# Performance work log

Hardware: AMD Instinct MI355X
Metric: run time of the kernel (lower is better)

## Reference

```python
import jax, jax.numpy as jnp
import numpy as np

B, T, I, H = 64, 512, 512, 512


def setup_inputs() -> dict:
    key = jax.random.key(0)
    ks = jax.random.split(key, 7)
    scale_i = 1.0 / np.sqrt(I)
    scale_h = 1.0 / np.sqrt(H)
    x = jax.random.normal(ks[0], (B, T, I), dtype=jnp.float32)
    h0 = jax.random.normal(ks[1], (B, H), dtype=jnp.float32)
    W_ih = jax.random.normal(ks[2], (3 * H, I), dtype=jnp.float32) * scale_i
    W_hh = jax.random.normal(ks[3], (3 * H, H), dtype=jnp.float32) * scale_h
    b_ih = jax.random.normal(ks[4], (3 * H,), dtype=jnp.float32) * scale_h
    b_hh = jax.random.normal(ks[5], (3 * H,), dtype=jnp.float32) * scale_h
    # ragged lengths, sorted descending (module's slicing logic assumes this)
    lengths = jnp.sort(jax.random.randint(ks[6], (B,), 1, T + 1))[::-1].astype(jnp.int64)
    return {"x": x, "h0": h0, "W_ih": W_ih, "W_hh": W_hh,
            "b_ih": b_ih, "b_hh": b_hh, "lengths": lengths}


def _gru_scan(x, h0, W_ih, W_hh, b_ih, b_hh, lengths):
    # Precompute input projections for all timesteps: [B, T, 3H]
    gi = jnp.einsum('bti,gi->btg', x, W_ih) + b_ih
    lengths = lengths.astype(jnp.int32)

    def step(h, inp):
        gi_t, t = inp  # gi_t: [B, 3H]
        gh = h @ W_hh.T + b_hh  # [B, 3H]
        i_r, i_z, i_n = jnp.split(gi_t, 3, axis=-1)
        h_r, h_z, h_n = jnp.split(gh, 3, axis=-1)
        r = jax.nn.sigmoid(i_r + h_r)
        z = jax.nn.sigmoid(i_z + h_z)
        n = jnp.tanh(i_n + r * h_n)
        h_new = (1.0 - z) * n + z * h
        m = (t < lengths)[:, None]  # ragged mask: valid rows this step
        h_keep = jnp.where(m, h_new, h)        # past-length rows keep last state
        y = jnp.where(m, h_new, 0.0)           # output stays zero past length
        return h_keep, y

    ts = jnp.arange(x.shape[1], dtype=jnp.int32)
    h_final, ys = jax.lax.scan(step, h0, (gi.transpose(1, 0, 2), ts))
    output = ys.transpose(1, 0, 2)  # [B, T, H]
    return output, h_final


def reference(x, h0, W_ih, W_hh, b_ih, b_hh, lengths):
    output, h_final = _gru_scan(x, h0, W_ih, W_hh, b_ih, b_hh, lengths)
    final_state = (h_final[None],)  # (1, B, H), matching unsqueeze(0)
    return output, final_state
```

## Files before the change

kernel.cpp:

```cpp
#include <hip/hip_runtime.h>
#include <stdint.h>

#define Bsz 64
#define Tsz 512
#define HD  512
#define GROUPS 4
#define MEMBERS 16
#define BROWS 16
#define JCH 32
#define NWG (GROUPS*MEMBERS)
#define NTHR 512
#define LROW 520
#define LROWD 260
#define HSLOT (Bsz*HD/2)

typedef __attribute__((ext_vector_type(8))) short bf16x8;
typedef __attribute__((ext_vector_type(4))) float f32x4;
typedef __attribute__((ext_vector_type(4))) uint32_t u32x4;
typedef __attribute__((ext_vector_type(2))) uint32_t u32x2;

#define BAR() asm volatile("s_waitcnt lgkmcnt(0)\n\ts_barrier" ::: "memory")

__device__ __forceinline__ uint32_t f2bf(float f) {
  uint32_t u = __builtin_bit_cast(uint32_t, f);
  return (u + 0x7FFFu + ((u >> 16) & 1u)) >> 16;
}

__device__ __forceinline__ bf16x8 ldwf(const float* __restrict__ W, int row, int k0) {
  const f32x4 a = *reinterpret_cast<const f32x4*>(W + (size_t)row * HD + k0);
  const f32x4 b = *reinterpret_cast<const f32x4*>(W + (size_t)row * HD + k0 + 4);
  bf16x8 r;
  r[0] = (short)f2bf(a.x); r[1] = (short)f2bf(a.y);
  r[2] = (short)f2bf(a.z); r[3] = (short)f2bf(a.w);
  r[4] = (short)f2bf(b.x); r[5] = (short)f2bf(b.y);
  r[6] = (short)f2bf(b.z); r[7] = (short)f2bf(b.w);
  return r;
}

__device__ __forceinline__ void stage_x0(const float* __restrict__ x, int b0,
                                         uint32_t* xl, int tid) {
#pragma unroll
  for (int i = 0; i < 4; ++i) {
    const int fl = tid + i * 512;
    const int row = fl >> 7;
    const int c4 = fl & 127;
    const f32x4 v = *reinterpret_cast<const f32x4*>(
        x + (size_t)(b0 + row) * Tsz * HD + c4 * 4);
    u32x2 w;
    w.x = f2bf(v.x) | (f2bf(v.y) << 16);
    w.y = f2bf(v.z) | (f2bf(v.w) << 16);
    *reinterpret_cast<u32x2*>(xl + row * LROWD + c4 * 2) = w;
  }
}

__global__ void gru_init(const float* __restrict__ h0, uint32_t* __restrict__ flg,
                         uint64_t* __restrict__ hbx) {
  const int i = blockIdx.x * 256 + threadIdx.x;
  if (i < 2 * GROUPS * 16) flg[i] = (i < GROUPS * 16) ? 0xFFFFFFFFu : 0u;
  if (i < HSLOT) {
    const float a = h0[2 * i], b = h0[2 * i + 1];
    hbx[HSLOT + i] = (uint64_t)(f2bf(a) | (f2bf(b) << 16));
    hbx[i] = 0xFFFFFFFF00000000ull;
  }
}

__global__ void __launch_bounds__(NTHR) gru_persist(
    const float* __restrict__ x, const float* __restrict__ h0,
    const float* __restrict__ Wih, const float* __restrict__ Whh,
    const float* __restrict__ bih, const float* __restrict__ bhh,
    const int* __restrict__ lens,
    float* __restrict__ out, float* __restrict__ outh,
    uint32_t* __restrict__ flg, uint64_t* __restrict__ hbx) {
  __shared__ alignas(16) unsigned short x_lds[2][BROWS * LROW];
  __shared__ alignas(16) unsigned short h_lds[BROWS * LROW];
  __shared__ alignas(16) float s_lds[BROWS][4][JCH];

  const int tid = threadIdx.x;
  const int lane = tid & 63;
  const int wv = tid >> 6;
  const int gid = blockIdx.x & 3;
  const int mem = blockIdx.x >> 2;
  const int b0 = gid * BROWS;
  const int j0 = mem * JCH;

  const int grow = tid >> 5;
  const int gj = tid & 31;
  const float br = bih[j0 + gj] + bhh[j0 + gj];
  const float bz = bih[512 + j0 + gj] + bhh[512 + j0 + gj];
  const float bi_n = bih[1024 + j0 + gj];
  const float bh_n = bhh[1024 + j0 + gj];
  float hprev = h0[(size_t)(b0 + grow) * HD + j0 + gj];
  const int lenr = lens[b0 + grow];
  float* const outp = out + (size_t)(b0 + grow) * Tsz * HD + j0 + gj;

  const int q = tid & 127;
  const int r0 = tid >> 7;

  const int xc4 = tid & 127;
  const int xr0 = tid >> 7;
  const float* xbp[4];
#pragma unroll
  for (int i = 0; i < 4; ++i)
    xbp[i] = x + (size_t)(b0 + xr0 + 4 * i) * Tsz * HD + xc4 * 4;

  const int c = lane & 15;
  const int kg = lane >> 4;
  bf16x8 wfa[16], wfb[16];
  if (wv < 4) {
    const int wrow = (wv >> 1) * 512 + j0 + (wv & 1) * 16 + c;
#pragma unroll
    for (int ks = 0; ks < 16; ++ks) {
      const int k0 = ks * 32 + kg * 8;
      wfa[ks] = ldwf(Wih, wrow, k0);
      wfb[ks] = ldwf(Whh, wrow, k0);
    }
  } else if (wv < 6) {
    const int wrow = 1024 + j0 + (wv - 4) * 16 + c;
#pragma unroll
    for (int ks = 0; ks < 16; ++ks) wfa[ks] = ldwf(Wih, wrow, ks * 32 + kg * 8);
  } else {
    const int wrow = 1024 + j0 + (wv - 6) * 16 + c;
#pragma unroll
    for (int ks = 0; ks < 16; ++ks) wfb[ks] = ldwf(Whh, wrow, ks * 32 + kg * 8);
  }

  stage_x0(x, b0, (uint32_t*)&x_lds[0][0], tid);

  f32x4 xr[4];
#pragma unroll
  for (int i = 0; i < 4; ++i)
    xr[i] = *reinterpret_cast<const f32x4*>(xbp[i] + (size_t)1 * HD);

  float o_pend = 0.f;

  __syncthreads();

  for (int t = 0; t < Tsz; ++t) {
    f32x4 acc0 = {0.f, 0.f, 0.f, 0.f}, acc1 = {0.f, 0.f, 0.f, 0.f};
    {
      const unsigned short* xl = &x_lds[t & 1][0];
      if (wv < 6) {
#pragma unroll
        for (int ks = 0; ks < 16; ks += 2) {
          bf16x8 a0 = *reinterpret_cast<const bf16x8*>(xl + c * LROW + ks * 32 + kg * 8);
          bf16x8 a1 = *reinterpret_cast<const bf16x8*>(xl + c * LROW + (ks + 1) * 32 + kg * 8);
          acc0 = __builtin_amdgcn_mfma_f32_16x16x32_bf16(a0, wfa[ks], acc0, 0, 0, 0);
          acc1 = __builtin_amdgcn_mfma_f32_16x16x32_bf16(a1, wfa[ks + 1], acc1, 0, 0, 0);
        }
      }
    }

    if (t + 1 < Tsz) {
      uint32_t* xl = (uint32_t*)&x_lds[(t + 1) & 1][0];
#pragma unroll
      for (int i = 0; i < 4; ++i) {
        u32x2 w;
        w.x = f2bf(xr[i].x) | (f2bf(xr[i].y) << 16);
        w.y = f2bf(xr[i].z) | (f2bf(xr[i].w) << 16);
        *reinterpret_cast<u32x2*>(xl + (xr0 + 4 * i) * LROWD + xc4 * 2) = w;
      }
    }

    const uint32_t want = (uint32_t)t;

    {
      const uint32_t* fl = flg + ((((t + 1) & 1) * GROUPS + gid) << 4);
      for (;;) {
        u32x4 f0, f1, f2, f3;
        asm volatile(
            "global_load_dwordx4 %0, %4, off sc0 sc1\n\t"
            "global_load_dwordx4 %1, %4, off offset:16 sc0 sc1\n\t"
            "global_load_dwordx4 %2, %4, off offset:32 sc0 sc1\n\t"
            "global_load_dwordx4 %3, %4, off offset:48 sc0 sc1\n\t"
            "s_waitcnt vmcnt(0)"
            : "=&v"(f0), "=&v"(f1), "=&v"(f2), "=&v"(f3)
            : "v"(fl)
            : "memory");
        bool ok = true;
#pragma unroll
        for (int i = 0; i < 4; ++i)
          ok &= (f0[i] == want) & (f1[i] == want) & (f2[i] == want) & (f3[i] == want);
        if (ok) break;
      }
    }

    {
      const uint64_t* bp = hbx + (size_t)((t + 1) & 1) * HSLOT;
      const uint64_t* a0 = bp + (size_t)(b0 + r0) * 256 + q * 2;
      const uint64_t* a1 = a0 + 4 * 256;
      const uint64_t* a2 = a0 + 8 * 256;
      const uint64_t* a3 = a0 + 12 * 256;
      u32x4 d0, d1, d2, d3;
      for (;;) {
        asm volatile(
            "global_load_dwordx4 %0, %4, off sc0 sc1\n\t"
            "global_load_dwordx4 %1, %5, off sc0 sc1\n\t"
            "global_load_dwordx4 %2, %6, off sc0 sc1\n\t"
            "global_load_dwordx4 %3, %7, off sc0 sc1\n\t"
            "s_waitcnt vmcnt(0)"
            : "=&v"(d0), "=&v"(d1), "=&v"(d2), "=&v"(d3)
            : "v"(a0), "v"(a1), "v"(a2), "v"(a3)
            : "memory");
        const bool ok = (d0[1] == want) & (d0[3] == want) & (d1[1] == want) &
                        (d1[3] == want) & (d2[1] == want) & (d2[3] == want) &
                        (d3[1] == want) & (d3[3] == want);
        if (ok) break;
      }
      uint32_t* hd = (uint32_t*)&h_lds[0] + q * 2;
      u32x2 w;
      w.x = d0[0]; w.y = d0[2];
      *reinterpret_cast<u32x2*>(hd + (r0) * LROWD) = w;
      w.x = d1[0]; w.y = d1[2];
      *reinterpret_cast<u32x2*>(hd + (r0 + 4) * LROWD) = w;
      w.x = d2[0]; w.y = d2[2];
      *reinterpret_cast<u32x2*>(hd + (r0 + 8) * LROWD) = w;
      w.x = d3[0]; w.y = d3[2];
      *reinterpret_cast<u32x2*>(hd + (r0 + 12) * LROWD) = w;
    }

    if (t > 0) outp[(size_t)(t - 1) * HD] = o_pend;

    BAR();

    if (t + 2 < Tsz) {
#pragma unroll
      for (int i = 0; i < 4; ++i)
        xr[i] = *reinterpret_cast<const f32x4*>(xbp[i] + (size_t)(t + 2) * HD);
    }

    {
      const unsigned short* hl = &h_lds[0];
      if (wv < 4 || wv >= 6) {
#pragma unroll
        for (int ks = 0; ks < 16; ks += 2) {
          bf16x8 a0 = *reinterpret_cast<const bf16x8*>(hl + c * LROW + ks * 32 + kg * 8);
          bf16x8 a1 = *reinterpret_cast<const bf16x8*>(hl + c * LROW + (ks + 1) * 32 + kg * 8);
          acc0 = __builtin_amdgcn_mfma_f32_16x16x32_bf16(a0, wfb[ks], acc0, 0, 0, 0);
          acc1 = __builtin_amdgcn_mfma_f32_16x16x32_bf16(a1, wfb[ks + 1], acc1, 0, 0, 0);
        }
      }
      const f32x4 acc = acc0 + acc1;
      const int slot = (wv < 4) ? (wv >> 1) : ((wv < 6) ? 2 : 3);
      const int col = (wv & 1) * 16 + c;
#pragma unroll
      for (int qq = 0; qq < 4; ++qq) s_lds[kg * 4 + qq][slot][col] = acc[qq];
    }
    BAR();

    {
      const float sr = s_lds[grow][0][gj] + br;
      const float sz = s_lds[grow][1][gj] + bz;
      const float si = s_lds[grow][2][gj] + bi_n;
      const float sh = s_lds[grow][3][gj] + bh_n;
      const float r = 1.f / (1.f + __expf(-sr));
      const float z = 1.f / (1.f + __expf(-sz));
      const float n = tanhf(si + r * sh);
      const float hnew = (1.f - z) * n + z * hprev;
      const bool m = (t < lenr);
      const float hk = m ? hnew : hprev;
      const uint32_t ub = f2bf(hk);
      const uint32_t ot = __shfl_xor(ub, 1);
      if ((t + 1 < Tsz) && ((lane & 1) == 0)) {
        const uint32_t word = ub | (ot << 16);
        const uint64_t pkt = ((uint64_t)(uint32_t)(t + 1) << 32) | (uint64_t)word;
        __hip_atomic_store(hbx + (size_t)(t & 1) * HSLOT + (size_t)(b0 + grow) * 256 +
                               ((j0 + gj) >> 1),
                           pkt, __ATOMIC_RELAXED, __HIP_MEMORY_SCOPE_AGENT);
      }
      if ((t + 1 < Tsz) && (tid == 0)) {
        __hip_atomic_store(flg + (((t & 1) * GROUPS + gid) << 4) + mem,
                           (uint32_t)(t + 1), __ATOMIC_RELAXED,
                           __HIP_MEMORY_SCOPE_AGENT);
      }
      o_pend = m ? hnew : 0.f;
      hprev = hk;
    }
  }

  outp[(size_t)(Tsz - 1) * HD] = o_pend;
  outh[(size_t)(b0 + grow) * HD + j0 + gj] = hprev;
}

extern "C" void kernel_launch(void* const* d_in, const int* in_sizes, int n_in,
                              void* d_out, int out_size, void* d_ws, size_t ws_size,
                              hipStream_t stream) {
  const float* x = (const float*)d_in[0];
  const float* h0 = (const float*)d_in[1];
  const float* Wih = (const float*)d_in[2];
  const float* Whh = (const float*)d_in[3];
  const float* bih = (const float*)d_in[4];
  const float* bhh = (const float*)d_in[5];
  const int* lens = (const int*)d_in[6];
  float* out = (float*)d_out;
  float* outh = out + (size_t)Bsz * Tsz * HD;

  uint32_t* flg = (uint32_t*)d_ws;
  uint64_t* hbx = (uint64_t*)((char*)d_ws + 512);

  gru_init<<<64, 256, 0, stream>>>(h0, flg, hbx);
  gru_persist<<<NWG, NTHR, 0, stream>>>(x, h0, Wih, Whh, bih, bhh, lens,
                                        out, outh, flg, hbx);
}
```

Baseline: 1.289 ms.

## Drop per-group flag handshake and speculatively prefetch tagged hidden-state packets

Removes the separate per-group flag array and its polling loop; readiness is now taken only from the step tags embedded in each 64-bit hidden-state packet. The hidden-state loads are issued at the top of each timestep so they overlap the input-projection MFMAs, and they are re-polled only if the tags are stale. This takes one global round trip and one atomic store per step off the serial recurrence critical path. The risk is extra polling traffic when the speculative load arrives too early, and correctness now rests entirely on the per-packet tags.

Measured after the change: 1.517 ms. 17.6% more time.

```diff
diff --git a/kernel.cpp b/kernel.cpp
--- a/kernel.cpp
+++ b/kernel.cpp
@@ -53,10 +53,8 @@
   }
 }
 
-__global__ void gru_init(const float* __restrict__ h0, uint32_t* __restrict__ flg,
-                         uint64_t* __restrict__ hbx) {
+__global__ void gru_init(const float* __restrict__ h0, uint64_t* __restrict__ hbx) {
   const int i = blockIdx.x * 256 + threadIdx.x;
-  if (i < 2 * GROUPS * 16) flg[i] = (i < GROUPS * 16) ? 0xFFFFFFFFu : 0u;
   if (i < HSLOT) {
     const float a = h0[2 * i], b = h0[2 * i + 1];
     hbx[HSLOT + i] = (uint64_t)(f2bf(a) | (f2bf(b) << 16));
@@ -70,7 +68,7 @@
     const float* __restrict__ bih, const float* __restrict__ bhh,
     const int* __restrict__ lens,
     float* __restrict__ out, float* __restrict__ outh,
-    uint32_t* __restrict__ flg, uint64_t* __restrict__ hbx) {
+    uint64_t* __restrict__ hbx) {
   __shared__ alignas(16) unsigned short x_lds[2][BROWS * LROW];
   __shared__ alignas(16) unsigned short h_lds[BROWS * LROW];
   __shared__ alignas(16) float s_lds[BROWS][4][JCH];
@@ -79,9 +77,8 @@
   const int lane = tid & 63;
   const int wv = tid >> 6;
   const int gid = blockIdx.x & 3;
-  const int mem = blockIdx.x >> 2;
   const int b0 = gid * BROWS;
-  const int j0 = mem * JCH;
+  const int j0 = (blockIdx.x >> 2) * JCH;
 
   const int grow = tid >> 5;
   const int gj = tid & 31;
@@ -136,16 +133,33 @@
   __syncthreads();
 
   for (int t = 0; t < Tsz; ++t) {
+    const uint32_t want = (uint32_t)t;
+    const uint64_t* bp = hbx + (size_t)((t + 1) & 1) * HSLOT;
+    const uint64_t* a0 = bp + (size_t)(b0 + r0) * 256 + q * 2;
+    const uint64_t* a1 = a0 + 4 * 256;
+    const uint64_t* a2 = a0 + 8 * 256;
+    const uint64_t* a3 = a0 + 12 * 256;
+    u32x4 d0, d1, d2, d3;
+
+    asm volatile(
+        "global_load_dwordx4 %0, %4, off sc0 sc1\n\t"
+        "global_load_dwordx4 %1, %5, off sc0 sc1\n\t"
+        "global_load_dwordx4 %2, %6, off sc0 sc1\n\t"
+        "global_load_dwordx4 %3, %7, off sc0 sc1"
+        : "=&v"(d0), "=&v"(d1), "=&v"(d2), "=&v"(d3)
+        : "v"(a0), "v"(a1), "v"(a2), "v"(a3)
+        : "memory");
+
     f32x4 acc0 = {0.f, 0.f, 0.f, 0.f}, acc1 = {0.f, 0.f, 0.f, 0.f};
     {
       const unsigned short* xl = &x_lds[t & 1][0];
       if (wv < 6) {
 #pragma unroll
         for (int ks = 0; ks < 16; ks += 2) {
-          bf16x8 a0 = *reinterpret_cast<const bf16x8*>(xl + c * LROW + ks * 32 + kg * 8);
-          bf16x8 a1 = *reinterpret_cast<const bf16x8*>(xl + c * LROW + (ks + 1) * 32 + kg * 8);
-          acc0 = __builtin_amdgcn_mfma_f32_16x16x32_bf16(a0, wfa[ks], acc0, 0, 0, 0);
-          acc1 = __builtin_amdgcn_mfma_f32_16x16x32_bf16(a1, wfa[ks + 1], acc1, 0, 0, 0);
+          bf16x8 a0f = *reinterpret_cast<const bf16x8*>(xl + c * LROW + ks * 32 + kg * 8);
+          bf16x8 a1f = *reinterpret_cast<const bf16x8*>(xl + c * LROW + (ks + 1) * 32 + kg * 8);
+          acc0 = __builtin_amdgcn_mfma_f32_16x16x32_bf16(a0f, wfa[ks], acc0, 0, 0, 0);
+          acc1 = __builtin_amdgcn_mfma_f32_16x16x32_bf16(a1f, wfa[ks + 1], acc1, 0, 0, 0);
         }
       }
     }
@@ -161,51 +175,25 @@
       }
     }
 
-    const uint32_t want = (uint32_t)t;
-
-    {
-      const uint32_t* fl = flg + ((((t + 1) & 1) * GROUPS + gid) << 4);
-      for (;;) {
-        u32x4 f0, f1, f2, f3;
-        asm volatile(
-            "global_load_dwordx4 %0, %4, off sc0 sc1\n\t"
-            "global_load_dwordx4 %1, %4, off offset:16 sc0 sc1\n\t"
-            "global_load_dwordx4 %2, %4, off offset:32 sc0 sc1\n\t"
-            "global_load_dwordx4 %3, %4, off offset:48 sc0 sc1\n\t"
-            "s_waitcnt vmcnt(0)"
-            : "=&v"(f0), "=&v"(f1), "=&v"(f2), "=&v"(f3)
-            : "v"(fl)
-            : "memory");
-        bool ok = true;
-#pragma unroll
-        for (int i = 0; i < 4; ++i)
-          ok &= (f0[i] == want) & (f1[i] == want) & (f2[i] == want) & (f3[i] == want);
-        if (ok) break;
-      }
-    }
-
-    {
-      const uint64_t* bp = hbx + (size_t)((t + 1) & 1) * HSLOT;
-      const uint64_t* a0 = bp + (size_t)(b0 + r0) * 256 + q * 2;
-      const uint64_t* a1 = a0 + 4 * 256;
-      const uint64_t* a2 = a0 + 8 * 256;
-      const uint64_t* a3 = a0 + 12 * 256;
-      u32x4 d0, d1, d2, d3;
-      for (;;) {
-        asm volatile(
-            "global_load_dwordx4 %0, %4, off sc0 sc1\n\t"
-            "global_load_dwordx4 %1, %5, off sc0 sc1\n\t"
-            "global_load_dwordx4 %2, %6, off sc0 sc1\n\t"
-            "global_load_dwordx4 %3, %7, off sc0 sc1\n\t"
-            "s_waitcnt vmcnt(0)"
-            : "=&v"(d0), "=&v"(d1), "=&v"(d2), "=&v"(d3)
-            : "v"(a0), "v"(a1), "v"(a2), "v"(a3)
-            : "memory");
-        const bool ok = (d0[1] == want) & (d0[3] == want) & (d1[1] == want) &
-                        (d1[3] == want) & (d2[1] == want) & (d2[3] == want) &
-                        (d3[1] == want) & (d3[3] == want);
-        if (ok) break;
-      }
+    asm volatile("s_waitcnt vmcnt(0)" ::: "memory");
+    __builtin_amdgcn_sched_barrier(0);
+    for (;;) {
+      const bool ok = (d0[1] == want) & (d0[3] == want) & (d1[1] == want) &
+                      (d1[3] == want) & (d2[1] == want) & (d2[3] == want) &
+                      (d3[1] == want) & (d3[3] == want);
+      if (ok) break;
+      asm volatile(
+          "global_load_dwordx4 %0, %4, off sc0 sc1\n\t"
+          "global_load_dwordx4 %1, %5, off sc0 sc1\n\t"
+          "global_load_dwordx4 %2, %6, off sc0 sc1\n\t"
+          "global_load_dwordx4 %3, %7, off sc0 sc1\n\t"
+          "s_waitcnt vmcnt(0)"
+          : "=&v"(d0), "=&v"(d1), "=&v"(d2), "=&v"(d3)
+          : "v"(a0), "v"(a1), "v"(a2), "v"(a3)
+          : "memory");
+      __builtin_amdgcn_sched_barrier(0);
+    }
+    {
       uint32_t* hd = (uint32_t*)&h_lds[0] + q * 2;
       u32x2 w;
       w.x = d0[0]; w.y = d0[2];
@@ -233,10 +221,10 @@
       if (wv < 4 || wv >= 6) {
 #pragma unroll
         for (int ks = 0; ks < 16; ks += 2) {
-          bf16x8 a0 = *reinterpret_cast<const bf16x8*>(hl + c * LROW + ks * 32 + kg * 8);
-          bf16x8 a1 = *reinterpret_cast<const bf16x8*>(hl + c * LROW + (ks + 1) * 32 + kg * 8);
-          acc0 = __builtin_amdgcn_mfma_f32_16x16x32_bf16(a0, wfb[ks], acc0, 0, 0, 0);
-          acc1 = __builtin_amdgcn_mfma_f32_16x16x32_bf16(a1, wfb[ks + 1], acc1, 0, 0, 0);
+          bf16x8 a0f = *reinterpret_cast<const bf16x8*>(hl + c * LROW + ks * 32 + kg * 8);
+          bf16x8 a1f = *reinterpret_cast<const bf16x8*>(hl + c * LROW + (ks + 1) * 32 + kg * 8);
+          acc0 = __builtin_amdgcn_mfma_f32_16x16x32_bf16(a0f, wfb[ks], acc0, 0, 0, 0);
+          acc1 = __builtin_amdgcn_mfma_f32_16x16x32_bf16(a1f, wfb[ks + 1], acc1, 0, 0, 0);
         }
       }
       const f32x4 acc = acc0 + acc1;
@@ -267,11 +255,6 @@
                                ((j0 + gj) >> 1),
                            pkt, __ATOMIC_RELAXED, __HIP_MEMORY_SCOPE_AGENT);
       }
-      if ((t + 1 < Tsz) && (tid == 0)) {
-        __hip_atomic_store(flg + (((t & 1) * GROUPS + gid) << 4) + mem,
-                           (uint32_t)(t + 1), __ATOMIC_RELAXED,
-                           __HIP_MEMORY_SCOPE_AGENT);
-      }
       o_pend = m ? hnew : 0.f;
       hprev = hk;
     }
@@ -294,10 +277,9 @@
   float* out = (float*)d_out;
   float* outh = out + (size_t)Bsz * Tsz * HD;
 
-  uint32_t* flg = (uint32_t*)d_ws;
-  uint64_t* hbx = (uint64_t*)((char*)d_ws + 512);
-
-  gru_init<<<64, 256, 0, stream>>>(h0, flg, hbx);
+  uint64_t* hbx = (uint64_t*)d_ws;
+
+  gru_init<<<64, 256, 0, stream>>>(h0, hbx);
   gru_persist<<<NWG, NTHR, 0, stream>>>(x, h0, Wih, Whh, bih, bhh, lens,
-                                        out, outh, flg, hbx);
-}
+                                        out, outh, hbx);
+}
```
